# Optimization experiments

Measured on AMD Instinct MI355X. Metric: run time of the kernel, lower is better.

Reference implementation:

```python
import jax, jax.numpy as jnp
import numpy as np
import math

D_MODEL = 768
N_HEADS = 12
B, S = 2, 2048


def setup_inputs() -> dict:
    key = jax.random.key(0)
    ks = jax.random.split(key, 12)
    q = jax.random.normal(ks[0], (B, S, D_MODEL), dtype=jnp.float32)
    k = jax.random.normal(ks[1], (B, S, D_MODEL), dtype=jnp.float32)
    v = jax.random.normal(ks[2], (B, S, D_MODEL), dtype=jnp.float32)
    # 2D causal mask (0 = masked), exercising the mask.dim()==2 branch
    mask = jnp.tril(jnp.ones((S, S), dtype=jnp.int32))
    sc = 1.0 / math.sqrt(D_MODEL)
    wq = jax.random.normal(ks[3], (D_MODEL, D_MODEL), dtype=jnp.float32) * sc
    wk = jax.random.normal(ks[4], (D_MODEL, D_MODEL), dtype=jnp.float32) * sc
    wv = jax.random.normal(ks[5], (D_MODEL, D_MODEL), dtype=jnp.float32) * sc
    wo = jax.random.normal(ks[6], (D_MODEL, D_MODEL), dtype=jnp.float32) * sc
    bq = jnp.zeros((D_MODEL,), jnp.float32)
    bk = jnp.zeros((D_MODEL,), jnp.float32)
    bv = jnp.zeros((D_MODEL,), jnp.float32)
    bo = jnp.zeros((D_MODEL,), jnp.float32)
    return {"query": q, "key": k, "value": v, "mask": mask,
            "wq": wq, "bq": bq, "wk": wk, "bk": bk,
            "wv": wv, "bv": bv, "wo": wo, "bo": bo}


def reference(query, key, value, mask, wq, bq, wk, bk, wv, bv, wo, bo):
    b, sq, d = query.shape
    h = N_HEADS
    dk = d // h
    scale = math.sqrt(dk)

    def proj(x, w, bias):  # torch Linear: x @ W^T + b, then split heads -> [b,h,s,dk]
        y = x @ w.T + bias
        return y.reshape(b, -1, h, dk).transpose(0, 2, 1, 3)

    Q = proj(query, wq, bq)
    K = proj(key, wk, bk)
    V = proj(value, wv, bv)

    scores = jnp.einsum('bhqd,bhkd->bhqk', Q, K) / scale  # [b,h,sq,sk]
    scores = jnp.where(mask[None, None, :, :] == 0, jnp.float32(-1e9), scores)
    attn = jax.nn.softmax(scores, axis=-1)  # dropout p=0 (eval): identity
    ctx = jnp.einsum('bhqk,bhkd->bhqd', attn, V)
    ctx = ctx.transpose(0, 2, 1, 3).reshape(b, sq, d)
    out = ctx @ wo.T + bo
    return out, attn
```

## Files before the change

kernel.cpp:

```cpp
#include <hip/hip_runtime.h>

#define D_MODEL 768
#define N_HEADS 12
#define DK      64
#define BB      2
#define SS      2048
#define PH      (BB*SS*D_MODEL)
#define WN      (D_MODEL*D_MODEL)

typedef short bf8_t   __attribute__((ext_vector_type(8)));
typedef float f32x4   __attribute__((ext_vector_type(4)));

__device__ __forceinline__ unsigned short f2b(float f) {
  unsigned u = __builtin_bit_cast(unsigned, f);
  unsigned r = (u + 0x7FFFu + ((u >> 16) & 1u)) >> 16;
  return (unsigned short)r;
}
__device__ __forceinline__ unsigned pk2(float a, float b) {
  return (unsigned)f2b(a) | ((unsigned)f2b(b) << 16);
}
__device__ __forceinline__ f32x4 mfma16(bf8_t a, bf8_t b, f32x4 c) {
  return __builtin_amdgcn_mfma_f32_16x16x32_bf16(a, b, c, 0, 0, 0);
}

__device__ __forceinline__ bf8_t ld_frag64(const unsigned short* t, int rbase, int kk, int lane) {
  int row = rbase + (lane & 15);
  int k = (kk << 5) + ((lane >> 4) << 3);
  uint4 u = *(const uint4*)&t[(row << 6) + (k ^ ((row & 7) << 3))];
  return __builtin_bit_cast(bf8_t, u);
}

__device__ __forceinline__ void st_tile_pair(unsigned short* lds, int r0, int k8, uint4 a0, uint4 a1) {
  int sw = ((k8 ^ (r0 & 7)) << 3);
  *(uint4*)&lds[(r0 << 6) + sw] = a0;
  *(uint4*)&lds[((r0 + 32) << 6) + sw] = a1;
}

__device__ __forceinline__ void mma_step(const unsigned short* As, const unsigned short* Ws,
                                         int w, int lane, f32x4 acc[4]) {
#pragma unroll
  for (int kk = 0; kk < 2; ++kk) {
    bf8_t a = ld_frag64(As, w << 4, kk, lane);
#pragma unroll
    for (int n = 0; n < 4; ++n)
      acc[n] = mfma16(a, ld_frag64(Ws, n << 4, kk, lane), acc[n]);
  }
}

__global__ __launch_bounds__(256)
void prep(const float* __restrict__ q, const float* __restrict__ k, const float* __restrict__ v,
          const float* __restrict__ wq, const float* __restrict__ wk,
          const float* __restrict__ wv, const float* __restrict__ wo,
          unsigned short* __restrict__ dst) {
  const int QKV_C = PH / 8;
  const int W_C   = WN / 8;
  const int TOTAL = 3 * QKV_C + 4 * W_C;
  for (int c = blockIdx.x * 256 + threadIdx.x; c < TOTAL; c += gridDim.x * 256) {
    const float* s;
    int off;
    if (c < 3 * QKV_C) {
      int seg = c / QKV_C; off = c - seg * QKV_C;
      s = seg == 0 ? q : seg == 1 ? k : v;
    } else {
      int c2 = c - 3 * QKV_C;
      int seg = c2 / W_C; off = c2 - seg * W_C;
      s = seg == 0 ? wq : seg == 1 ? wk : seg == 2 ? wv : wo;
    }
    const float* p = s + (size_t)off * 8;
    float4 a = *(const float4*)p;
    float4 b = *(const float4*)(p + 4);
    uint4 o;
    o.x = pk2(a.x, a.y); o.y = pk2(a.z, a.w);
    o.z = pk2(b.x, b.y); o.w = pk2(b.z, b.w);
    *(uint4*)&dst[(size_t)c * 8] = o;
  }
}

__global__ __launch_bounds__(256)
void qkv_proj(const unsigned short* __restrict__ Qc, const unsigned short* __restrict__ Kc,
              const unsigned short* __restrict__ Vc,
              const unsigned short* __restrict__ Wq, const unsigned short* __restrict__ Wk,
              const unsigned short* __restrict__ Wv,
              const float* __restrict__ bq, const float* __restrict__ bk,
              const float* __restrict__ bv,
              unsigned short* __restrict__ Qh, unsigned short* __restrict__ Kh,
              unsigned short* __restrict__ VT) {
  __shared__ __align__(16) unsigned short As[4096];
  __shared__ __align__(16) unsigned short Ws[4096];
  const int tid = threadIdx.x, lane = tid & 63, w = tid >> 6;
  const int g = lane >> 4, qc = lane & 15;
  const int p = blockIdx.x;
  const int l = (p & 7) * 288 + (p >> 3);
  const int z = l / 768, rr = l % 768;
  const int m0 = (rr / 12) << 6, n0 = (rr % 12) << 6;

  const unsigned short* A = z == 0 ? Qc : z == 1 ? Kc : Vc;
  const unsigned short* W = z == 0 ? Wq : z == 1 ? Wk : Wv;
  const float* bias = z == 0 ? bq : z == 1 ? bk : bv;
  const float oscale = z == 0 ? 0.125f : 1.0f;

  const int r0 = tid >> 3, k8 = tid & 7;
  const unsigned short* Ab0 = A + (size_t)(m0 + r0) * D_MODEL + (k8 << 3);
  const unsigned short* Ab1 = Ab0 + 32 * D_MODEL;
  const unsigned short* Wb0 = W + (size_t)(n0 + r0) * D_MODEL + (k8 << 3);
  const unsigned short* Wb1 = Wb0 + 32 * D_MODEL;

  uint4 ra0 = *(const uint4*)Ab0, ra1 = *(const uint4*)Ab1;
  uint4 rw0 = *(const uint4*)Wb0, rw1 = *(const uint4*)Wb1;

  f32x4 acc[4] = {};
  for (int kt = 0; kt < 12; ++kt) {
    __syncthreads();
    st_tile_pair(As, r0, k8, ra0, ra1);
    st_tile_pair(Ws, r0, k8, rw0, rw1);
    __syncthreads();
    if (kt < 11) {
      int off = (kt + 1) << 6;
      ra0 = *(const uint4*)(Ab0 + off); ra1 = *(const uint4*)(Ab1 + off);
      rw0 = *(const uint4*)(Wb0 + off); rw1 = *(const uint4*)(Wb1 + off);
    }
    mma_step(As, Ws, w, lane, acc);
  }

  const int wrow = (w << 4) + (g << 2);
  const int b = m0 >> 11;
  const int h = n0 >> 6;
  if (z < 2) {
    unsigned short* dst = (z == 0 ? Qh : Kh) + ((size_t)(b * N_HEADS + h)) * SS * DK;
#pragma unroll
    for (int n = 0; n < 4; ++n) {
      int col = (n << 4) + qc;
      float bb = bias[n0 + col];
#pragma unroll
      for (int r = 0; r < 4; ++r) {
        int s = (m0 + wrow + r) & (SS - 1);
        dst[(size_t)s * DK + col] = f2b((acc[n][r] + bb) * oscale);
      }
    }
  } else {
    unsigned short* dst = VT + ((size_t)(b * N_HEADS + h)) * DK * SS;
#pragma unroll
    for (int n = 0; n < 4; ++n) {
      int col = (n << 4) + qc;
      float bb = bias[n0 + col];
      int s = (m0 + wrow) & (SS - 1);
      ushort4 pk;
      pk.x = f2b(acc[n][0] + bb); pk.y = f2b(acc[n][1] + bb);
      pk.z = f2b(acc[n][2] + bb); pk.w = f2b(acc[n][3] + bb);
      *(ushort4*)&dst[(size_t)col * SS + s] = pk;
    }
  }
}

__global__ __launch_bounds__(256)
void attn2(const unsigned short* __restrict__ Qh, const unsigned short* __restrict__ Kh,
           const unsigned short* __restrict__ VT,
           float* __restrict__ attn, unsigned short* __restrict__ ctx) {
  __shared__ __align__(16) unsigned short Ks[4096];
  __shared__ __align__(16) unsigned short Vts[4096];
  __shared__ __align__(16) unsigned short Pw[4][1024];

  const int tid = threadIdx.x, lane = tid & 63, w = tid >> 6;
  const int g = lane >> 4, qc = lane & 15;
  const int p = blockIdx.x;
  const int l = (p & 7) * 96 + (p >> 3);
  const int bh = l >> 5;
  const int x = l & 31;
  const int qt = (x & 1) ? (31 - (x >> 1)) : (x >> 1);
  const int q0 = qt << 6;
  const int b = bh / N_HEADS, h = bh - b * N_HEADS;

  const unsigned short* Qb = Qh + (size_t)bh * SS * DK;
  const unsigned short* Kb = Kh + (size_t)bh * SS * DK;
  const unsigned short* Vb = VT + (size_t)bh * DK * SS;
  float* attn_b = attn + (size_t)bh * SS * SS;

  bf8_t qf0, qf1;
  {
    const unsigned short* qp = &Qb[(size_t)(q0 + (w << 4) + (lane & 15)) * DK + (g << 3)];
    qf0 = __builtin_bit_cast(bf8_t, *(const uint4*)qp);
    qf1 = __builtin_bit_cast(bf8_t, *(const uint4*)(qp + 32));
  }

  const int r0 = tid >> 3, k8 = tid & 7;
  auto ldK = [&](int t, uint4& a0, uint4& a1) {
    const unsigned short* bse = Kb + ((size_t)t << 12);
    a0 = *(const uint4*)&bse[(r0 << 6) + (k8 << 3)];
    a1 = *(const uint4*)&bse[((r0 + 32) << 6) + (k8 << 3)];
  };
  auto ldV = [&](int t, uint4& a0, uint4& a1) {
    const unsigned short* bse = Vb + (t << 6);
    a0 = *(const uint4*)&bse[(size_t)r0 * SS + (k8 << 3)];
    a1 = *(const uint4*)&bse[(size_t)(r0 + 32) * SS + (k8 << 3)];
  };

  const int wrow = (w << 4) + (g << 2);
  float l_acc[4] = {0.f, 0.f, 0.f, 0.f};

  {
    uint4 ka0, ka1;
    ldK(0, ka0, ka1);
    for (int t = 0; t <= qt; ++t) {
      __syncthreads();
      st_tile_pair(Ks, r0, k8, ka0, ka1);
      __syncthreads();
      if (t < qt) ldK(t + 1, ka0, ka1);
      f32x4 sc[4] = {};
#pragma unroll
      for (int kk = 0; kk < 2; ++kk) {
        bf8_t a = kk ? qf1 : qf0;
#pragma unroll
        for (int n = 0; n < 4; ++n)
          sc[n] = mfma16(a, ld_frag64(Ks, n << 4, kk, lane), sc[n]);
      }
      const bool diag = (t == qt);
      float part[4] = {0.f, 0.f, 0.f, 0.f};
#pragma unroll
      for (int n = 0; n < 4; ++n) {
        int col = (n << 4) + qc;
#pragma unroll
        for (int r = 0; r < 4; ++r) {
          bool ok = !diag || (col <= wrow + r);
          part[r] += ok ? __expf(sc[n][r]) : 0.f;
        }
      }
#pragma unroll
      for (int r = 0; r < 4; ++r) {
        float s = part[r];
        s += __shfl_xor(s, 1);
        s += __shfl_xor(s, 2);
        s += __shfl_xor(s, 4);
        s += __shfl_xor(s, 8);
        l_acc[r] += s;
      }
    }
  }

  float Linv[4];
#pragma unroll
  for (int r = 0; r < 4; ++r) Linv[r] = 1.0f / l_acc[r];

  f32x4 ct[4] = {};
  unsigned short* myP = Pw[w];
  {
    uint4 ka0, ka1, va0, va1;
    ldK(0, ka0, ka1);
    ldV(0, va0, va1);
    for (int t = 0; t <= qt; ++t) {
      __syncthreads();
      st_tile_pair(Ks, r0, k8, ka0, ka1);
      st_tile_pair(Vts, r0, k8, va0, va1);
      __syncthreads();
      if (t < qt) { ldK(t + 1, ka0, ka1); ldV(t + 1, va0, va1); }
      f32x4 sc[4] = {};
#pragma unroll
      for (int kk = 0; kk < 2; ++kk) {
        bf8_t a = kk ? qf1 : qf0;
#pragma unroll
        for (int n = 0; n < 4; ++n)
          sc[n] = mfma16(a, ld_frag64(Ks, n << 4, kk, lane), sc[n]);
      }
      const bool diag = (t == qt);
      const int k0 = t << 6;
#pragma unroll
      for (int n = 0; n < 4; ++n) {
        int col = (n << 4) + qc;
#pragma unroll
        for (int r = 0; r < 4; ++r) {
          bool ok = !diag || (col <= wrow + r);
          float pv = ok ? __expf(sc[n][r]) * Linv[r] : 0.f;
          attn_b[(size_t)(q0 + wrow + r) * SS + k0 + col] = pv;
          int prow = (g << 2) + r;
          myP[(prow << 6) + (col ^ ((prow & 7) << 3))] = f2b(pv);
        }
      }
      asm volatile("s_waitcnt lgkmcnt(0)" ::: "memory");
      __builtin_amdgcn_sched_barrier(0);
#pragma unroll
      for (int kk = 0; kk < 2; ++kk) {
        bf8_t pf = ld_frag64(myP, 0, kk, lane);
#pragma unroll
        for (int n = 0; n < 4; ++n)
          ct[n] = mfma16(pf, ld_frag64(Vts, n << 4, kk, lane), ct[n]);
      }
    }
  }

  {
    const int zr = tid >> 4;
    const int zc = (tid & 15) << 2;
    const float4 z4 = {0.f, 0.f, 0.f, 0.f};
    for (int c0 = q0 + 64; c0 < SS; c0 += 64) {
#pragma unroll
      for (int i = 0; i < 4; ++i)
        *(float4*)&attn_b[(size_t)(q0 + zr + (i << 4)) * SS + c0 + zc] = z4;
    }
  }

#pragma unroll
  for (int n = 0; n < 4; ++n) {
#pragma unroll
    for (int r = 0; r < 4; ++r) {
      int m = q0 + wrow + r;
      int col = (n << 4) + qc;
      ctx[((size_t)(b * SS + m)) * D_MODEL + h * DK + col] = f2b(ct[n][r]);
    }
  }
}

__global__ __launch_bounds__(256)
void out_proj(const unsigned short* __restrict__ A, const unsigned short* __restrict__ W,
              const float* __restrict__ bias, float* __restrict__ out) {
  __shared__ __align__(16) unsigned short As[4096];
  __shared__ __align__(16) unsigned short Ws[4096];
  const int tid = threadIdx.x, lane = tid & 63, w = tid >> 6;
  const int g = lane >> 4, qc = lane & 15;
  const int p = blockIdx.x;
  const int l = (p & 7) * 96 + (p >> 3);
  const int m0 = (l / 12) << 6, n0 = (l % 12) << 6;

  const int r0 = tid >> 3, k8 = tid & 7;
  const unsigned short* Ab0 = A + (size_t)(m0 + r0) * D_MODEL + (k8 << 3);
  const unsigned short* Ab1 = Ab0 + 32 * D_MODEL;
  const unsigned short* Wb0 = W + (size_t)(n0 + r0) * D_MODEL + (k8 << 3);
  const unsigned short* Wb1 = Wb0 + 32 * D_MODEL;

  uint4 ra0 = *(const uint4*)Ab0, ra1 = *(const uint4*)Ab1;
  uint4 rw0 = *(const uint4*)Wb0, rw1 = *(const uint4*)Wb1;

  f32x4 acc[4] = {};
  for (int kt = 0; kt < 12; ++kt) {
    __syncthreads();
    st_tile_pair(As, r0, k8, ra0, ra1);
    st_tile_pair(Ws, r0, k8, rw0, rw1);
    __syncthreads();
    if (kt < 11) {
      int off = (kt + 1) << 6;
      ra0 = *(const uint4*)(Ab0 + off); ra1 = *(const uint4*)(Ab1 + off);
      rw0 = *(const uint4*)(Wb0 + off); rw1 = *(const uint4*)(Wb1 + off);
    }
    mma_step(As, Ws, w, lane, acc);
  }

  const int wrow = (w << 4) + (g << 2);
#pragma unroll
  for (int n = 0; n < 4; ++n) {
    int col = n0 + (n << 4) + qc;
    float bb = bias[col];
#pragma unroll
    for (int r = 0; r < 4; ++r)
      out[(size_t)(m0 + wrow + r) * D_MODEL + col] = acc[n][r] + bb;
  }
}

extern "C" void kernel_launch(void* const* d_in, const int* in_sizes, int n_in,
                              void* d_out, int out_size, void* d_ws, size_t ws_size,
                              hipStream_t stream) {
  const float* q  = (const float*)d_in[0];
  const float* k  = (const float*)d_in[1];
  const float* v  = (const float*)d_in[2];
  const float* wq = (const float*)d_in[4];
  const float* bq = (const float*)d_in[5];
  const float* wk = (const float*)d_in[6];
  const float* bk = (const float*)d_in[7];
  const float* wv = (const float*)d_in[8];
  const float* bv = (const float*)d_in[9];
  const float* wo = (const float*)d_in[10];
  const float* bo = (const float*)d_in[11];

  float* out  = (float*)d_out;
  float* attn = out + (size_t)BB * SS * D_MODEL;

  unsigned short* wsu = (unsigned short*)d_ws;
  unsigned short* Qc  = wsu;
  unsigned short* Kc  = Qc + PH;
  unsigned short* Vc  = Kc + PH;
  unsigned short* Wqb = Vc + PH;
  unsigned short* Wkb = Wqb + WN;
  unsigned short* Wvb = Wkb + WN;
  unsigned short* Wob = Wvb + WN;
  unsigned short* Qhd = Wob + WN;
  unsigned short* Khd = Qhd + PH;
  unsigned short* VTw = Khd + PH;
  unsigned short* Cw  = VTw + PH;

  dim3 blk(256);
  prep<<<2048, blk, 0, stream>>>(q, k, v, wq, wk, wv, wo, wsu);
  qkv_proj<<<2304, blk, 0, stream>>>(Qc, Kc, Vc, Wqb, Wkb, Wvb, bq, bk, bv, Qhd, Khd, VTw);
  attn2<<<768, blk, 0, stream>>>(Qhd, Khd, VTw, attn, Cw);
  out_proj<<<768, blk, 0, stream>>>(Cw, Wob, bo, out);
}
```

Baseline: 171.8 us.

## Transpose score MFMA so lanes own key runs, vectorizing attn and P stores

```diff
diff --git a/kernel.cpp b/kernel.cpp
--- a/kernel.cpp
+++ b/kernel.cpp
@@ -153,7 +153,7 @@
 }
 
 __global__ __launch_bounds__(256)
-void attn2(const unsigned short* __restrict__ Qh, const unsigned short* __restrict__ Kh,
+void attn4(const unsigned short* __restrict__ Qh, const unsigned short* __restrict__ Kh,
            const unsigned short* __restrict__ VT,
            float* __restrict__ attn, unsigned short* __restrict__ ctx) {
   __shared__ __align__(16) unsigned short Ks[4096];
@@ -177,7 +177,7 @@
 
   bf8_t qf0, qf1;
   {
-    const unsigned short* qp = &Qb[(size_t)(q0 + (w << 4) + (lane & 15)) * DK + (g << 3)];
+    const unsigned short* qp = &Qb[(size_t)(q0 + (w << 4) + qc) * DK + (g << 3)];
     qf0 = __builtin_bit_cast(bf8_t, *(const uint4*)qp);
     qf1 = __builtin_bit_cast(bf8_t, *(const uint4*)(qp + 32));
   }
@@ -194,8 +194,8 @@
     a1 = *(const uint4*)&bse[(size_t)(r0 + 32) * SS + (k8 << 3)];
   };
 
-  const int wrow = (w << 4) + (g << 2);
-  float l_acc[4] = {0.f, 0.f, 0.f, 0.f};
+  const int qglob = q0 + (w << 4) + qc;
+  float psum = 0.f;
 
   {
     uint4 ka0, ka1;
@@ -208,37 +208,27 @@
       f32x4 sc[4] = {};
 #pragma unroll
       for (int kk = 0; kk < 2; ++kk) {
-        bf8_t a = kk ? qf1 : qf0;
+        bf8_t qf = kk ? qf1 : qf0;
 #pragma unroll
         for (int n = 0; n < 4; ++n)
-          sc[n] = mfma16(a, ld_frag64(Ks, n << 4, kk, lane), sc[n]);
+          sc[n] = mfma16(ld_frag64(Ks, n << 4, kk, lane), qf, sc[n]);
       }
       const bool diag = (t == qt);
-      float part[4] = {0.f, 0.f, 0.f, 0.f};
+      const int kbase = (t << 6) + (g << 2);
 #pragma unroll
       for (int n = 0; n < 4; ++n) {
-        int col = (n << 4) + qc;
 #pragma unroll
         for (int r = 0; r < 4; ++r) {
-          bool ok = !diag || (col <= wrow + r);
-          part[r] += ok ? __expf(sc[n][r]) : 0.f;
+          int k = kbase + (n << 4) + r;
+          bool ok = !diag || (k <= qglob);
+          psum += ok ? __expf(sc[n][r]) : 0.f;
         }
       }
-#pragma unroll
-      for (int r = 0; r < 4; ++r) {
-        float s = part[r];
-        s += __shfl_xor(s, 1);
-        s += __shfl_xor(s, 2);
-        s += __shfl_xor(s, 4);
-        s += __shfl_xor(s, 8);
-        l_acc[r] += s;
-      }
-    }
-  }
-
-  float Linv[4];
-#pragma unroll
-  for (int r = 0; r < 4; ++r) Linv[r] = 1.0f / l_acc[r];
+    }
+  }
+  psum += __shfl_xor(psum, 16);
+  psum += __shfl_xor(psum, 32);
+  const float Linv = 1.0f / psum;
 
   f32x4 ct[4] = {};
   unsigned short* myP = Pw[w];
@@ -255,24 +245,30 @@
       f32x4 sc[4] = {};
 #pragma unroll
       for (int kk = 0; kk < 2; ++kk) {
-        bf8_t a = kk ? qf1 : qf0;
+        bf8_t qf = kk ? qf1 : qf0;
 #pragma unroll
         for (int n = 0; n < 4; ++n)
-          sc[n] = mfma16(a, ld_frag64(Ks, n << 4, kk, lane), sc[n]);
+          sc[n] = mfma16(ld_frag64(Ks, n << 4, kk, lane), qf, sc[n]);
       }
       const bool diag = (t == qt);
       const int k0 = t << 6;
 #pragma unroll
       for (int n = 0; n < 4; ++n) {
-        int col = (n << 4) + qc;
+        int klocal = (n << 4) + (g << 2);
+        int kb = k0 + klocal;
+        float pr[4];
 #pragma unroll
         for (int r = 0; r < 4; ++r) {
-          bool ok = !diag || (col <= wrow + r);
-          float pv = ok ? __expf(sc[n][r]) * Linv[r] : 0.f;
-          attn_b[(size_t)(q0 + wrow + r) * SS + k0 + col] = pv;
-          int prow = (g << 2) + r;
-          myP[(prow << 6) + (col ^ ((prow & 7) << 3))] = f2b(pv);
+          bool ok = !diag || (kb + r <= qglob);
+          pr[r] = ok ? __expf(sc[n][r]) * Linv : 0.f;
         }
+        float4 pv;
+        pv.x = pr[0]; pv.y = pr[1]; pv.z = pr[2]; pv.w = pr[3];
+        *(float4*)&attn_b[(size_t)qglob * SS + kb] = pv;
+        uint2 pk;
+        pk.x = pk2(pr[0], pr[1]);
+        pk.y = pk2(pr[2], pr[3]);
+        *(uint2*)&myP[(qc << 6) + (klocal ^ ((qc & 7) << 3))] = pk;
       }
       asm volatile("s_waitcnt lgkmcnt(0)" ::: "memory");
       __builtin_amdgcn_sched_barrier(0);
@@ -297,6 +293,7 @@
     }
   }
 
+  const int wrow = (w << 4) + (g << 2);
 #pragma unroll
   for (int n = 0; n < 4; ++n) {
 #pragma unroll
@@ -387,6 +384,6 @@
   dim3 blk(256);
   prep<<<2048, blk, 0, stream>>>(q, k, v, wq, wk, wv, wo, wsu);
   qkv_proj<<<2304, blk, 0, stream>>>(Qc, Kc, Vc, Wqb, Wkb, Wvb, bq, bk, bv, Qhd, Khd, VTw);
-  attn2<<<768, blk, 0, stream>>>(Qhd, Khd, VTw, attn, Cw);
+  attn4<<<768, blk, 0, stream>>>(Qhd, Khd, VTw, attn, Cw);
   out_proj<<<768, blk, 0, stream>>>(Cw, Wob, bo, out);
 }
```

After: 172.0 us. Within noise of the previous version (+0.1%).
